# Optimization experiments

Measured on AMD Instinct MI355X. Metric: run time of the kernel, lower is better.

Reference implementation:

```python
import jax, jax.numpy as jnp
import numpy as np

B, T_ENC, T_DEC = 32, 256, 256
ENC, HID, ATT, CCH, K = 512, 1024, 128, 32, 31
OUT, PRE = 80, 256
ZONEOUT = 0.1
P_DROP = 0.5
PAD = (K - 1) // 2


def setup_inputs() -> dict:
    key = jax.random.key(0)
    ks = jax.random.split(key, 20)
    def n(k, shape, s=0.02):
        return jax.random.normal(k, shape, dtype=jnp.float32) * s
    inp = {}
    inp["encoder_outs"] = jax.random.normal(ks[0], (B, T_ENC, ENC), dtype=jnp.float32)
    inp["decoder_targets"] = jax.random.normal(ks[1], (B, T_DEC, OUT), dtype=jnp.float32)
    keep = 1.0 - P_DROP
    # pre-sampled inverted-dropout masks for the 2 prenet layers at every step
    inp["prenet_masks"] = jax.random.bernoulli(ks[2], keep, (T_DEC, 2, B, PRE)).astype(jnp.float32) / keep
    inp["in_lens"] = jax.random.randint(ks[3], (B,), T_ENC // 2, T_ENC + 1, dtype=jnp.int32)
    # location-sensitive attention params
    inp["V_w"] = n(ks[4], (ATT, ENC)); inp["V_b"] = jnp.zeros((ATT,), jnp.float32)
    inp["W_w"] = n(ks[5], (ATT, HID))
    inp["U_w"] = n(ks[6], (ATT, CCH))
    inp["F_w"] = n(ks[7], (CCH, 1, K))
    inp["w_w"] = n(ks[8], (1, ATT)); inp["w_b"] = jnp.zeros((1,), jnp.float32)
    # prenet
    inp["pre_w0"] = n(ks[9], (PRE, OUT)); inp["pre_b0"] = jnp.zeros((PRE,), jnp.float32)
    inp["pre_w1"] = n(ks[10], (PRE, PRE)); inp["pre_b1"] = jnp.zeros((PRE,), jnp.float32)
    # stacked LSTM cells (zoneout wrappers)
    inp["l0_wih"] = n(ks[11], (4 * HID, ENC + PRE)); inp["l0_whh"] = n(ks[12], (4 * HID, HID))
    inp["l0_bih"] = jnp.zeros((4 * HID,), jnp.float32); inp["l0_bhh"] = jnp.zeros((4 * HID,), jnp.float32)
    inp["l1_wih"] = n(ks[13], (4 * HID, HID)); inp["l1_whh"] = n(ks[14], (4 * HID, HID))
    inp["l1_bih"] = jnp.zeros((4 * HID,), jnp.float32); inp["l1_bhh"] = jnp.zeros((4 * HID,), jnp.float32)
    # output projections
    inp["feat_w"] = n(ks[15], (OUT, ENC + HID))
    inp["prob_w"] = n(ks[16], (1, ENC + HID)); inp["prob_b"] = jnp.zeros((1,), jnp.float32)
    return inp


def _lstm_cell(x, h, c, wih, whh, bih, bhh):
    g = x @ wih.T + bih + h @ whh.T + bhh
    i, f, gg, o = jnp.split(g, 4, axis=1)  # torch LSTMCell gate order
    c2 = jax.nn.sigmoid(f) * c + jax.nn.sigmoid(i) * jnp.tanh(gg)
    h2 = jax.nn.sigmoid(o) * jnp.tanh(c2)
    return h2, c2


def _decode(encoder_outs, decoder_targets, prenet_masks, in_lens,
            V_w, V_b, W_w, U_w, F_w, w_w, w_b,
            pre_w0, pre_b0, pre_w1, pre_b1,
            l0_wih, l0_whh, l0_bih, l0_bhh,
            l1_wih, l1_whh, l1_bih, l1_bhh,
            feat_w, prob_w, prob_b):
    b = encoder_outs.shape[0]
    pad_mask = jnp.arange(T_ENC)[None, :] >= in_lens[:, None]       # [B,T_enc] True = pad
    att_uniform = (~pad_mask).astype(jnp.float32) / in_lens[:, None].astype(jnp.float32)
    processed_memory = encoder_outs @ V_w.T + V_b                   # [B,T_enc,ATT]
    neg = jnp.float32(-1e9)

    # teacher forcing: prev_out at step 0 is the go-frame, then target[t-1]
    targets_prev = jnp.concatenate(
        [jnp.zeros((b, 1, OUT), jnp.float32), decoder_targets[:, :-1]], axis=1)
    xs = (jnp.swapaxes(targets_prev, 0, 1), prenet_masks[:, 0], prenet_masks[:, 1],
          jnp.arange(T_DEC))

    def step(carry, x):
        h0, c0, h1, c1, cum = carry
        prev_out, m0, m1, t = x
        # location-sensitive attention (prev_att_w = None at t=0 -> uniform over valid)
        att_prev = jnp.where(t == 0, att_uniform, cum)              # [B,T_enc]
        f = jax.lax.conv_general_dilated(
            att_prev[:, None, :], F_w, (1,), [(PAD, PAD)],
            dimension_numbers=("NCH", "OIH", "NCH"))                # [B,CCH,T_enc]
        f = jnp.swapaxes(f, 1, 2)                                   # [B,T_enc,CCH]
        erg = jnp.tanh(processed_memory + (h0 @ W_w.T)[:, None, :] + f @ U_w.T)
        erg = (erg @ w_w.T + w_b)[..., 0]                           # [B,T_enc]
        erg = jnp.where(pad_mask, neg, erg)
        aw = jax.nn.softmax(erg, axis=1)
        att_c = jnp.einsum("bt,bte->be", aw, encoder_outs)          # [B,ENC]
        # prenet (dropout always on, via pre-sampled masks)
        p = jax.nn.relu(prev_out @ pre_w0.T + pre_b0) * m0
        p = jax.nn.relu(p @ pre_w1.T + pre_b1) * m1
        xin = jnp.concatenate([att_c, p], axis=1)
        # zoneout LSTM stack (eval-mode zoneout: convex mix of prev/new states)
        h0n, c0n = _lstm_cell(xin, h0, c0, l0_wih, l0_whh, l0_bih, l0_bhh)
        h0 = ZONEOUT * h0 + (1.0 - ZONEOUT) * h0n
        c0 = ZONEOUT * c0 + (1.0 - ZONEOUT) * c0n
        h1n, c1n = _lstm_cell(h0, h1, c1, l1_wih, l1_whh, l1_bih, l1_bhh)
        h1 = ZONEOUT * h1 + (1.0 - ZONEOUT) * h1n
        c1 = ZONEOUT * c1 + (1.0 - ZONEOUT) * c1n
        hcs = jnp.concatenate([h1, att_c], axis=1)                  # [B,HID+ENC]
        out = hcs @ feat_w.T                                        # [B,OUT] (no bias)
        logit = hcs @ prob_w.T + prob_b                             # [B,1]
        return (h0, c0, h1, c1, cum + aw), (out, logit, aw)

    z = jnp.zeros((b, HID), jnp.float32)
    carry0 = (z, z, z, z, jnp.zeros((b, T_ENC), jnp.float32))
    _, (outs, logits, att_ws) = jax.lax.scan(step, carry0, xs)
    outs = jnp.transpose(outs, (1, 2, 0))      # [B,OUT,T_dec]
    logits = logits[..., 0].T                  # [B,T_dec]
    att_ws = jnp.swapaxes(att_ws, 0, 1)        # [B,T_dec,T_enc]
    return outs, logits, att_ws


def reference(encoder_outs, decoder_targets, prenet_masks, in_lens,
              V_w, V_b, W_w, U_w, F_w, w_w, w_b,
              pre_w0, pre_b0, pre_w1, pre_b1,
              l0_wih, l0_whh, l0_bih, l0_bhh,
              l1_wih, l1_whh, l1_bih, l1_bhh,
              feat_w, prob_w, prob_b):
    return _decode(encoder_outs, decoder_targets, prenet_masks, in_lens,
                   V_w, V_b, W_w, U_w, F_w, w_w, w_b,
                   pre_w0, pre_b0, pre_w1, pre_b1,
                   l0_wih, l0_whh, l0_bih, l0_bhh,
                   l1_wih, l1_whh, l1_bih, l1_bhh,
                   feat_w, prob_w, prob_b)
```

## Files before the change

### kernel.cpp

```cpp
#include <hip/hip_runtime.h>

typedef _Float16 half2_t __attribute__((ext_vector_type(2)));
typedef unsigned uint_t;

#define B_    32
#define TE_   256
#define TD_   256
#define ENC_  512
#define HID_  1024
#define ATT_  128
#define OUT_  80
#define PRE_  256

#define LOG_OFF  655360u
#define ATTW_OFF 663552u

#define OFF_PM    0u
#define OFF_P1H   1048576u
#define OFF_M     2097152u
#define OFF_WWHT  2101248u
#define OFF_ENCH  2166784u
#define OFF_W0P   4263936u
#define OFF_W1P   7933952u
#define OFF_XC0   12128256u
#define OFF_XC1   12173312u
#define OFF_C0    12206080u
#define OFF_C1    12238848u
#define OFF_CUM   12271616u
#define OFF_ATTC  12279808u
#define OFF_END   12328960u

__device__ __forceinline__ float rcp_f(float x){ return __builtin_amdgcn_rcpf(x); }
__device__ __forceinline__ float sigm(float x){ return rcp_f(1.0f + __expf(-x)); }
__device__ __forceinline__ float tanh_f(float x){ float e = __expf(2.0f*x); return 1.0f - 2.0f*rcp_f(e+1.0f); }

__device__ __forceinline__ uint_t packh2(float a, float b){
  half2_t h; h[0] = (_Float16)a; h[1] = (_Float16)b;
  return __builtin_bit_cast(uint_t, h);
}
__device__ __forceinline__ float dot2f(uint_t w, uint_t x, float c){
#if __has_builtin(__builtin_amdgcn_fdot2)
  return __builtin_amdgcn_fdot2(__builtin_bit_cast(half2_t, w),
                                __builtin_bit_cast(half2_t, x), c, false);
#else
  half2_t a = __builtin_bit_cast(half2_t, w), b = __builtin_bit_cast(half2_t, x);
  return c + (float)a[0]*(float)b[0] + (float)a[1]*(float)b[1];
#endif
}


__global__ void k_init(float* __restrict__ ws){
  unsigned n = OFF_END - OFF_XC0;
  for (unsigned i = blockIdx.x*blockDim.x + threadIdx.x; i < n; i += gridDim.x*blockDim.x)
    ws[OFF_XC0 + i] = 0.f;
}

__global__ void k_precm(const float* __restrict__ Uw, const float* __restrict__ Fw,
                        float* __restrict__ ws){
  float* M = ws + OFF_M;
  for (int idx = threadIdx.x; idx < 128*31; idx += blockDim.x){
    int a = idx / 31, k = idx % 31;
    float s = 0.f;
    for (int c = 0; c < 32; c++) s += Uw[a*32+c]*Fw[c*31+k];
    M[idx] = s;
  }
}

__global__ void k_cvtww(const float* __restrict__ Ww, float* __restrict__ ws){
  uint_t* WT = (uint_t*)(ws + OFF_WWHT);
  int p = blockIdx.x;
  for (int a = threadIdx.x; a < 128; a += blockDim.x)
    WT[p*128 + a] = packh2(Ww[a*1024 + 2*p], Ww[a*1024 + 2*p + 1]);
}

__global__ void k_packenc(const float* __restrict__ enc, float* __restrict__ ws){
  uint_t* ENCH = (uint_t*)(ws + OFF_ENCH);
  size_t row = blockIdx.x;
  for (int j = threadIdx.x; j < 256; j += blockDim.x)
    ENCH[row*256 + j] = packh2(enc[row*512 + 2*j], enc[row*512 + 2*j + 1]);
}

__global__ void k_packw0(const float* __restrict__ wih, const float* __restrict__ whh,
                         float* __restrict__ ws){
  uint_t* W = (uint_t*)(ws + OFF_W0P);
  size_t r = blockIdx.x;
  for (int p = threadIdx.x; p < 896; p += blockDim.x){
    int k = 2*p;
    const float* src = (k < 768) ? (wih + r*768 + k) : (whh + r*1024 + (k-768));
    W[r*896 + p] = packh2(src[0], src[1]);
  }
}

__global__ void k_packw1(const float* __restrict__ wih, const float* __restrict__ whh,
                         float* __restrict__ ws){
  uint_t* W = (uint_t*)(ws + OFF_W1P);
  size_t r = blockIdx.x;
  for (int p = threadIdx.x; p < 1024; p += blockDim.x){
    int k = 2*p;
    const float* src = (k < 1024) ? (wih + r*1024 + k) : (whh + r*1024 + (k-1024));
    W[r*1024 + p] = packh2(src[0], src[1]);
  }
}

__global__ __launch_bounds__(256) void k_pm(const float* __restrict__ enc,
    const float* __restrict__ Vw, const float* __restrict__ Vb, float* __restrict__ ws){
  float* pm = ws + OFF_PM;
  int b  = blockIdx.x >> 2;
  int s0 = (blockIdx.x & 3) << 6;
  int a  = threadIdx.x & 127;
  int sh = threadIdx.x >> 7;
  __shared__ float Vl[128*65];
  __shared__ float El[64*64];
  float acc[32];
  #pragma unroll
  for (int i=0;i<32;i++) acc[i]=0.f;
  for (int kc=0; kc<ENC_; kc+=64){
    for (int i=threadIdx.x; i<128*64; i+=256){
      int aa = i>>6, kk = i&63;
      Vl[aa*65+kk] = Vw[aa*ENC_ + kc + kk];
    }
    for (int i=threadIdx.x; i<64*64; i+=256){
      int ss = i>>6, kk = i&63;
      El[i] = enc[(size_t)(b*TE_ + s0 + ss)*ENC_ + kc + kk];
    }
    __syncthreads();
    for (int k=0;k<64;k++){
      float va = Vl[a*65+k];
      const float* er = &El[(sh*32)*64 + k];
      #pragma unroll
      for (int s=0;s<32;s++) acc[s] += va * er[s*64];
    }
    __syncthreads();
  }
  float bb = Vb[a];
  for (int s=0;s<32;s++)
    pm[((size_t)b*128 + a)*256 + (s0 + sh*32 + s)] = acc[s] + bb;
}

__global__ __launch_bounds__(256) void k_pre(const float* __restrict__ tgt,
    const float* __restrict__ w0, const float* __restrict__ b0,
    const float* __restrict__ w1, const float* __restrict__ b1,
    const float* __restrict__ masks, float* __restrict__ ws){
  uint_t* P1H = (uint_t*)(ws + OFF_P1H);
  int t = blockIdx.x, j = threadIdx.x;
  __shared__ float xl[32*80];
  __shared__ float p0l[32*256];
  __shared__ float p1s[256*32];
  for (int i=j; i<32*80; i+=256){
    int b = i/80, o = i%80;
    xl[i] = (t==0) ? 0.f : tgt[((size_t)b*TD_ + (t-1))*80 + o];
  }
  __syncthreads();
  {
    float bj = b0[j];
    float w[80];
    #pragma unroll
    for (int o=0;o<80;o++) w[o] = w0[j*80+o];
    for (int b=0;b<32;b++){
      float a0=0,a1=0,a2=0,a3=0;
      const float* x = &xl[b*80];
      #pragma unroll
      for (int o=0;o<80;o+=4){
        a0+=w[o]*x[o]; a1+=w[o+1]*x[o+1]; a2+=w[o+2]*x[o+2]; a3+=w[o+3]*x[o+3];
      }
      float m = masks[(((size_t)t*2+0)*32+b)*256 + j];
      p0l[b*256 + j] = fmaxf(bj+a0+a1+a2+a3, 0.f) * m;
    }
  }
  __syncthreads();
  {
    float bj = b1[j];
    const float4* wr = (const float4*)(w1 + j*256);
    float acc[32];
    #pragma unroll
    for (int i=0;i<32;i++) acc[i]=0.f;
    for (int o4=0;o4<64;o4++){
      float4 w = wr[o4];
      #pragma unroll
      for (int b=0;b<32;b++){
        const float4 xv = *(const float4*)&p0l[b*256 + o4*4];
        acc[b] += w.x*xv.x + w.y*xv.y + w.z*xv.z + w.w*xv.w;
      }
    }
    for (int b=0;b<32;b++){
      float m = masks[(((size_t)t*2+1)*32+b)*256 + j];
      p1s[j*32 + b] = fmaxf(bj+acc[b], 0.f) * m;
    }
  }
  __syncthreads();
  for (int i=j; i<32*128; i+=256){
    int b = i >> 7, jp = i & 127;
    P1H[((size_t)t*32 + b)*128 + jp] = packh2(p1s[(2*jp)*32 + b], p1s[(2*jp+1)*32 + b]);
  }
}


__global__ __launch_bounds__(512) void k_stepa(int t,
    const int* __restrict__ lens, const float* __restrict__ ww, const float* __restrict__ wb,
    const float* __restrict__ featw, const float* __restrict__ probw,
    const float* __restrict__ probb, float* __restrict__ ws, float* __restrict__ out){
  __shared__ __align__(16) uint_t h0l[512];
  __shared__ __align__(16) float Ml[128*32];
  __shared__ __align__(16) float apad[320];
  __shared__ __align__(16) float whl[128];
  __shared__ __align__(16) float wl[128];
  __shared__ __align__(16) float scl[256];
  __shared__ __align__(16) float awl[256];
  __shared__ __align__(16) float redl[128];
  __shared__ __align__(16) float psq[2048];
  __shared__ __align__(16) float redo[512];
  const int blk = blockIdx.x, tid = threadIdx.x;
  const int pc = t & 1, pp = pc ^ 1;
  uint_t* XC0 = (uint_t*)(ws + OFF_XC0);
  uint_t* XC1 = (uint_t*)(ws + OFF_XC1);
  float* ATTC = ws + OFF_ATTC;

  if (blk >= 32){
    if (t < 2) return;
    const int tt = t - 2;
    int ob = blk - 32;
    int b = tid & 31, rr = (tid>>5)&3, ksq = tid>>7;
    int r = ob*4 + rr;
    const float* wr = (r < 80) ? (featw + (size_t)r*1536) : probw;
    const float* acp = ATTC + (size_t)(tt%3)*16384 + b*512;
    float acc = 0.f;
    for (int j=0;j<96;j++){
      int k = ksq*384 + j*4;
      float x0,x1,x2,x3;
      if (k < 1024){
        uint2 hw = *(const uint2*)(XC1 + b*1024 + pc*512 + (k>>1));
        half2_t ha = __builtin_bit_cast(half2_t, hw.x);
        half2_t hb = __builtin_bit_cast(half2_t, hw.y);
        x0 = (float)ha[0]; x1 = (float)ha[1]; x2 = (float)hb[0]; x3 = (float)hb[1];
      } else {
        float4 f = *(const float4*)(acp + (k-1024));
        x0 = f.x; x1 = f.y; x2 = f.z; x3 = f.w;
      }
      if (r <= 80){
        float4 wv = *(const float4*)(wr + k);
        acc += wv.x*x0 + wv.y*x1 + wv.z*x2 + wv.w*x3;
      }
    }
    redo[(rr*4+ksq)*32 + b] = acc;
    __syncthreads();
    if (tid < 128){
      int b2 = tid&31, r2 = tid>>5;
      float vsum = redo[(r2*4+0)*32+b2] + redo[(r2*4+1)*32+b2]
                 + redo[(r2*4+2)*32+b2] + redo[(r2*4+3)*32+b2];
      int rr2 = ob*4 + r2;
      if (rr2 < 80)       out[((size_t)b2*80 + rr2)*256 + tt] = vsum;
      else if (rr2 == 80) out[LOG_OFF + (size_t)b2*256 + tt] = vsum + probb[0];
    }
    return;
  }

  if (t >= TD_) return;
  const int b = blk;
  const int len = lens[b];
  const float* PM = ws + OFF_PM;
  const float* Mg = ws + OFF_M;
  const uint_t* WWHT = (const uint_t*)(ws + OFF_WWHT);
  const uint_t* ENCH = (const uint_t*)(ws + OFF_ENCH);
  const uint_t* P1H = (const uint_t*)(ws + OFF_P1H);
  float* CUM = ws + OFF_CUM;

  if (tid < 128)
    *(uint4*)(h0l + tid*4) = *(const uint4*)(XC0 + b*1408 + 384 + pp*512 + tid*4);
  for (int i=tid; i<128*31; i+=512) Ml[(i/31)*32 + (i%31)] = Mg[i];
  for (int i=tid; i<288; i+=512){
    int p = i - 15;
    float vv = 0.f;
    if (p >= 0 && p < 256)
      vv = (t==0) ? ((p < len) ? 1.0f/(float)len : 0.f) : CUM[b*256 + p];
    apad[i] = vv;
  }
  if (tid < 128) wl[tid] = ww[tid];
  __syncthreads();
  {
    int aW = tid & 127, qW = tid >> 7;
    const uint_t* wt = WWHT + (size_t)(qW*128)*128 + aW;
    const uint_t* hb = h0l + qW*128;
    float s0 = 0.f, s1 = 0.f;
    #pragma unroll 8
    for (int p=0;p<128;p+=2){
      s0 = dot2f(wt[(size_t)p*128],     hb[p],   s0);
      s1 = dot2f(wt[(size_t)(p+1)*128], hb[p+1], s1);
    }
    psq[qW*128 + aW] = s0 + s1;
  }
  __syncthreads();
  if (tid < 128) whl[tid] = psq[tid] + psq[128+tid] + psq[256+tid] + psq[384+tid];
  __syncthreads();
  {
    int pg = tid & 63, q = tid >> 6;
    float apw[36];
    #pragma unroll
    for (int i=0;i<36;i+=4) *(float4*)&apw[i] = *(const float4*)&apad[pg*4 + i];
    float part0=0, part1=0, part2=0, part3=0;
    const float* pmb = PM + (size_t)b*128*256;
    for (int aa=0; aa<16; aa++){
      int a = q*16 + aa;
      const float* mr = Ml + a*32;
      float4 pv = *(const float4*)(pmb + (size_t)a*256 + pg*4);
      float wa = whl[a];
      float u0 = pv.x + wa, u1 = pv.y + wa, u2 = pv.z + wa, u3 = pv.w + wa;
      #pragma unroll
      for (int k=0;k<28;k+=4){
        float4 m4 = *(const float4*)(mr + k);
        u0 += m4.x*apw[k]   + m4.y*apw[k+1] + m4.z*apw[k+2] + m4.w*apw[k+3];
        u1 += m4.x*apw[k+1] + m4.y*apw[k+2] + m4.z*apw[k+3] + m4.w*apw[k+4];
        u2 += m4.x*apw[k+2] + m4.y*apw[k+3] + m4.z*apw[k+4] + m4.w*apw[k+5];
        u3 += m4.x*apw[k+3] + m4.y*apw[k+4] + m4.z*apw[k+5] + m4.w*apw[k+6];
      }
      float m28 = mr[28], m29 = mr[29], m30 = mr[30];
      u0 += m28*apw[28] + m29*apw[29] + m30*apw[30];
      u1 += m28*apw[29] + m29*apw[30] + m30*apw[31];
      u2 += m28*apw[30] + m29*apw[31] + m30*apw[32];
      u3 += m28*apw[31] + m29*apw[32] + m30*apw[33];
      float wv = wl[a];
      part0 += tanh_f(u0)*wv; part1 += tanh_f(u1)*wv;
      part2 += tanh_f(u2)*wv; part3 += tanh_f(u3)*wv;
    }
    float4 pp2; pp2.x = part0; pp2.y = part1; pp2.z = part2; pp2.w = part3;
    *(float4*)&psq[tid*4] = pp2;
  }
  __syncthreads();
  if (tid < 256){
    float s = wb[0];
    int pgg = tid >> 2, d = tid & 3;
    #pragma unroll
    for (int qq=0;qq<8;qq++) s += psq[(qq*64 + pgg)*4 + d];
    scl[tid] = (tid >= len) ? -1.0e9f : s;
  }
  __syncthreads();
  if (tid < 128) redl[tid] = fmaxf(scl[tid], scl[tid+128]);
  __syncthreads();
  if (tid < 64){
    float v = fmaxf(redl[tid], redl[tid+64]);
    #pragma unroll
    for (int off=32; off>0; off>>=1) v = fmaxf(v, __shfl_down(v, off));
    if (tid==0) redl[0] = v;
  }
  __syncthreads();
  float mx = redl[0];
  if (tid < 256) awl[tid] = __expf(scl[tid]-mx);
  __syncthreads();
  if (tid < 128) redl[tid] = awl[tid] + awl[tid+128];
  __syncthreads();
  if (tid < 64){
    float v = redl[tid] + redl[tid+64];
    #pragma unroll
    for (int off=32; off>0; off>>=1) v += __shfl_down(v, off);
    if (tid==0) redl[0] = v;
  }
  __syncthreads();
  float inv = rcp_f(redl[0]);
  if (tid < 256){
    float aw = awl[tid]*inv;
    awl[tid] = aw;
    CUM[b*256 + tid] += aw;
    out[ATTW_OFF + ((size_t)b*TD_ + t)*256 + tid] = aw;
  }
  __syncthreads();
  {
    int el = tid & 127, ph = tid >> 7;
    const uint_t* ep = ENCH + ((size_t)b*256 + ph*64)*256 + el*2;
    float c0=0,c1=0,c2=0,c3=0;
    for (int p=0;p<64;p++){
      float a = awl[ph*64 + p];
      uint2 ev = *(const uint2*)(ep + (size_t)p*256);
      half2_t h0v = __builtin_bit_cast(half2_t, ev.x);
      half2_t h1v = __builtin_bit_cast(half2_t, ev.y);
      c0 += a*(float)h0v[0]; c1 += a*(float)h0v[1];
      c2 += a*(float)h1v[0]; c3 += a*(float)h1v[1];
    }
    float4 ca; ca.x=c0; ca.y=c1; ca.z=c2; ca.w=c3;
    *(float4*)&psq[(ph*128 + el)*4] = ca;
  }
  __syncthreads();
  if (tid < 128){
    float4 s = *(const float4*)&psq[tid*4];
    #pragma unroll
    for (int g=1; g<4; g++){
      float4 o = *(const float4*)&psq[(g*128+tid)*4];
      s.x+=o.x; s.y+=o.y; s.z+=o.z; s.w+=o.w;
    }
    *(float4*)(ATTC + (size_t)(t%3)*16384 + b*512 + tid*4) = s;
    XC0[b*1408 + tid*2]     = packh2(s.x, s.y);
    XC0[b*1408 + tid*2 + 1] = packh2(s.z, s.w);
    XC0[b*1408 + 256 + tid] = P1H[((size_t)t*32 + b)*128 + tid];
  }
}


__global__ __launch_bounds__(512) void k_stepb(int t,
    const float* __restrict__ l0bih, const float* __restrict__ l0bhh,
    const float* __restrict__ l1bih, const float* __restrict__ l1bhh,
    float* __restrict__ ws){
  __shared__ __align__(16) uint_t lds[16*1028 + 32*132];
  uint_t* wlds = lds;
  uint_t* xl   = lds + 16*1028;
  float*  gs   = (float*)lds;
  const int tid = threadIdx.x;
  const int pc = t & 1, pp = pc ^ 1;
  const int bp = tid & 15, ul = (tid>>4)&3, kq = tid>>6;
  const int sb = tid >> 4, sp = (tid & 15) * 8;
  const bool is0 = blockIdx.x < 256;
  const int u0 = (is0 ? blockIdx.x : blockIdx.x - 256) * 4;
  uint_t* XC0 = (uint_t*)(ws + OFF_XC0);
  uint_t* XC1 = (uint_t*)(ws + OFF_XC1);
  _Float16* XC0h = (_Float16*)XC0;
  _Float16* XC1h = (_Float16*)XC1;

  if (is0){
    if (t >= TD_) return;
    const uint_t* W0P = (const uint_t*)(ws + OFF_W0P);
    for (int i=tid; i<16*896; i+=512){
      int r = i/896, p = i - r*896;
      wlds[r*904 + p] = W0P[(size_t)((r&3)*1024 + u0 + (r>>2))*896 + p];
    }
    float a0[4]={0,0,0,0}, a1[4]={0,0,0,0};
    uint4 rx0, rx1;
    { const uint_t* src = XC0 + sb*1408 + sp;
      rx0 = *(const uint4*)src; rx1 = *(const uint4*)(src+4); }
    #pragma unroll 1
    for (int c=0;c<7;c++){
      __syncthreads();
      *(uint4*)(xl + sb*132 + sp)     = rx0;
      *(uint4*)(xl + sb*132 + sp + 4) = rx1;
      __syncthreads();
      if (c+1 < 7){
        int co = (c+1)*128 + sp;
        const uint_t* src = (co < 384) ? (XC0 + sb*1408 + co)
                                       : (XC0 + sb*1408 + 384 + pp*512 + (co-384));
        rx0 = *(const uint4*)src; rx1 = *(const uint4*)(src+4);
      }
      const int wb = c*128 + kq*16;
      const uint_t* xpa = xl + bp*132 + kq*16;
      const uint_t* xpb = xl + (bp+16)*132 + kq*16;
      uint2 xa[8], xb[8];
      #pragma unroll
      for (int j=0;j<8;j++){ xa[j] = *(const uint2*)(xpa + 2*j); xb[j] = *(const uint2*)(xpb + 2*j); }
      #pragma unroll
      for (int g=0; g<4; g++){
        const uint_t* wr = wlds + (g + 4*ul)*904 + wb;
        float s0 = a0[g], s1 = a1[g];
        #pragma unroll
        for (int j=0;j<8;j++){
          uint2 w = *(const uint2*)(wr + 2*j);
          s0 = dot2f(w.x, xa[j].x, s0); s0 = dot2f(w.y, xa[j].y, s0);
          s1 = dot2f(w.x, xb[j].x, s1); s1 = dot2f(w.y, xb[j].y, s1);
        }
        a0[g] = s0; a1[g] = s1;
      }
    }
    __syncthreads();
    #pragma unroll
    for (int g=0; g<4; g++){
      gs[(kq*16 + g + 4*ul)*33 + bp]      = a0[g];
      gs[(kq*16 + g + 4*ul)*33 + bp + 16] = a1[g];
    }
    __syncthreads();
    if (tid < 128){
      int b = tid & 31, uu = tid >> 5;
      int u = u0 + uu;
      float g4[4];
      #pragma unroll
      for (int g=0; g<4; g++){
        float s = 0.f;
        #pragma unroll
        for (int k2=0;k2<8;k2++) s += gs[(k2*16 + g + 4*uu)*33 + b];
        g4[g] = s + l0bih[g*1024+u] + l0bhh[g*1024+u];
      }
      float c_old = (ws + OFF_C0)[u*32 + b];
      float h_old = (float)XC0h[b*2816 + 768 + pp*1024 + u];
      float cn = sigm(g4[1])*c_old + sigm(g4[0])*tanh_f(g4[2]);
      float hn = sigm(g4[3])*tanh_f(cn);
      (ws + OFF_C0)[u*32 + b] = 0.1f*c_old + 0.9f*cn;
      XC0h[b*2816 + 768 + pc*1024 + u] = (_Float16)(0.1f*h_old + 0.9f*hn);
    }
  } else {
    if (t < 1) return;
    const uint_t* W1P = (const uint_t*)(ws + OFF_W1P);
    for (int i=tid; i<16*1024; i+=512){
      int r = i >> 10, p = i & 1023;
      wlds[r*1028 + p] = W1P[(size_t)((r&3)*1024 + u0 + (r>>2))*1024 + p];
    }
    float a0[4]={0,0,0,0}, a1[4]={0,0,0,0};
    uint4 rx0, rx1;
    { const uint_t* src = XC0 + sb*1408 + 384 + pp*512 + sp;
      rx0 = *(const uint4*)src; rx1 = *(const uint4*)(src+4); }
    #pragma unroll 1
    for (int c=0;c<8;c++){
      __syncthreads();
      *(uint4*)(xl + sb*132 + sp)     = rx0;
      *(uint4*)(xl + sb*132 + sp + 4) = rx1;
      __syncthreads();
      if (c+1 < 8){
        int co = (c+1)*128 + sp;
        const uint_t* src = (co < 512) ? (XC0 + sb*1408 + 384 + pp*512 + co)
                                       : (XC1 + sb*1024 + pc*512 + (co-512));
        rx0 = *(const uint4*)src; rx1 = *(const uint4*)(src+4);
      }
      const int wb = c*128 + kq*16;
      const uint_t* xpa = xl + bp*132 + kq*16;
      const uint_t* xpb = xl + (bp+16)*132 + kq*16;
      uint2 xa[8], xb[8];
      #pragma unroll
      for (int j=0;j<8;j++){ xa[j] = *(const uint2*)(xpa + 2*j); xb[j] = *(const uint2*)(xpb + 2*j); }
      #pragma unroll
      for (int g=0; g<4; g++){
        const uint_t* wr = wlds + (g + 4*ul)*1028 + wb;
        float s0 = a0[g], s1 = a1[g];
        #pragma unroll
        for (int j=0;j<8;j++){
          uint2 w = *(const uint2*)(wr + 2*j);
          s0 = dot2f(w.x, xa[j].x, s0); s0 = dot2f(w.y, xa[j].y, s0);
          s1 = dot2f(w.x, xb[j].x, s1); s1 = dot2f(w.y, xb[j].y, s1);
        }
        a0[g] = s0; a1[g] = s1;
      }
    }
    __syncthreads();
    #pragma unroll
    for (int g=0; g<4; g++){
      gs[(kq*16 + g + 4*ul)*33 + bp]      = a0[g];
      gs[(kq*16 + g + 4*ul)*33 + bp + 16] = a1[g];
    }
    __syncthreads();
    if (tid < 128){
      int b = tid & 31, uu = tid >> 5;
      int u = u0 + uu;
      float g4[4];
      #pragma unroll
      for (int g=0; g<4; g++){
        float s = 0.f;
        #pragma unroll
        for (int k2=0;k2<8;k2++) s += gs[(k2*16 + g + 4*uu)*33 + b];
        g4[g] = s + l1bih[g*1024+u] + l1bhh[g*1024+u];
      }
      float c_old = (ws + OFF_C1)[u*32 + b];
      float h_old = (float)XC1h[b*2048 + pc*1024 + u];
      float cn = sigm(g4[1])*c_old + sigm(g4[0])*tanh_f(g4[2]);
      float hn = sigm(g4[3])*tanh_f(cn);
      (ws + OFF_C1)[u*32 + b] = 0.1f*c_old + 0.9f*cn;
      XC1h[b*2048 + pp*1024 + u] = (_Float16)(0.1f*h_old + 0.9f*hn);
    }
  }
}

extern "C" void kernel_launch(void* const* d_in, const int* in_sizes, int n_in,
                              void* d_out, int out_size, void* d_ws, size_t ws_size,
                              hipStream_t stream){
  const float* enc   = (const float*)d_in[0];
  const float* tgt   = (const float*)d_in[1];
  const float* masks = (const float*)d_in[2];
  const int*   lens  = (const int*)  d_in[3];
  const float* Vw    = (const float*)d_in[4];
  const float* Vb    = (const float*)d_in[5];
  const float* Ww    = (const float*)d_in[6];
  const float* Uw    = (const float*)d_in[7];
  const float* Fw    = (const float*)d_in[8];
  const float* ww    = (const float*)d_in[9];
  const float* wb    = (const float*)d_in[10];
  const float* pw0   = (const float*)d_in[11];
  const float* pb0   = (const float*)d_in[12];
  const float* pw1   = (const float*)d_in[13];
  const float* pb1   = (const float*)d_in[14];
  const float* l0wih = (const float*)d_in[15];
  const float* l0whh = (const float*)d_in[16];
  const float* l0bih = (const float*)d_in[17];
  const float* l0bhh = (const float*)d_in[18];
  const float* l1wih = (const float*)d_in[19];
  const float* l1whh = (const float*)d_in[20];
  const float* l1bih = (const float*)d_in[21];
  const float* l1bhh = (const float*)d_in[22];
  const float* featw = (const float*)d_in[23];
  const float* probw = (const float*)d_in[24];
  const float* probb = (const float*)d_in[25];
  float* ws  = (float*)d_ws;
  float* out = (float*)d_out;

  k_init   <<<256, 256,0,stream>>>(ws);
  k_pre    <<<256, 256,0,stream>>>(tgt, pw0, pb0, pw1, pb1, masks, ws);
  k_precm  <<<1,   256,0,stream>>>(Uw, Fw, ws);
  k_cvtww  <<<512, 128,0,stream>>>(Ww, ws);
  k_packenc<<<8192,256,0,stream>>>(enc, ws);
  k_packw0 <<<4096,256,0,stream>>>(l0wih, l0whh, ws);
  k_packw1 <<<4096,256,0,stream>>>(l1wih, l1whh, ws);
  k_pm     <<<128, 256,0,stream>>>(enc, Vw, Vb, ws);

  for (int t = 0; t < TD_; t++){
    k_stepa<<<56, 512,0,stream>>>(t, lens, ww, wb, featw, probw, probb, ws, out);
    k_stepb<<<512,512,0,stream>>>(t, l0bih, l0bhh, l1bih, l1bhh, ws);
  }
  k_stepb<<<512,512,0,stream>>>(256, l0bih, l0bhh, l1bih, l1bhh, ws);
  k_stepa<<<56, 512,0,stream>>>(256, lens, ww, wb, featw, probw, probb, ws, out);
  k_stepa<<<56, 512,0,stream>>>(257, lens, ww, wb, featw, probw, probb, ws, out);
}
```

Before: 15.92 ms.

## Merge LSTM layer blocks into one block and prefetch weights into registers

The separate layer-0 and layer-1 LSTM blocks become one block per 4 hidden units that runs both layers in turn, halving the grid to 256 blocks. All weights for both layers, along with biases and old cell and hidden states, are loaded into registers at kernel start so the global loads overlap. The activation chunks are double-buffered in LDS with a two-ahead register prefetch, which removes one barrier per chunk, and the LDS reads are widened to 128 bits. In exchange each block does serial work for both layers and carries heavy register pressure (15 uint4 of weights per thread), with launch bounds set to one block per CU.

```diff
diff --git a/kernel.cpp b/kernel.cpp
--- a/kernel.cpp
+++ b/kernel.cpp
@@ -393,67 +393,125 @@
 }
 
 
-__global__ __launch_bounds__(512) void k_stepb(int t,
+#define W0S 908
+#define W1S 1028
+#define LW1 14528u
+#define LXB0 30976u
+#define LXB1 35200u
+#define LTOT 39424u
+
+__global__ __launch_bounds__(512, 1) void k_stepb(int t,
     const float* __restrict__ l0bih, const float* __restrict__ l0bhh,
     const float* __restrict__ l1bih, const float* __restrict__ l1bhh,
     float* __restrict__ ws){
-  __shared__ __align__(16) uint_t lds[16*1028 + 32*132];
-  uint_t* wlds = lds;
-  uint_t* xl   = lds + 16*1028;
-  float*  gs   = (float*)lds;
+  __shared__ __align__(16) uint_t lds[LTOT];
+  uint_t* w0l = lds;
+  uint_t* w1l = lds + LW1;
+  float*  gs  = (float*)(lds + LW1);
   const int tid = threadIdx.x;
   const int pc = t & 1, pp = pc ^ 1;
   const int bp = tid & 15, ul = (tid>>4)&3, kq = tid>>6;
-  const int sb = tid >> 4, sp = (tid & 15) * 8;
-  const bool is0 = blockIdx.x < 256;
-  const int u0 = (is0 ? blockIdx.x : blockIdx.x - 256) * 4;
+  const int sb = tid >> 4, sp = (tid & 15)*8;
+  const int u0 = blockIdx.x*4;
   uint_t* XC0 = (uint_t*)(ws + OFF_XC0);
   uint_t* XC1 = (uint_t*)(ws + OFF_XC1);
   _Float16* XC0h = (_Float16*)XC0;
   _Float16* XC1h = (_Float16*)XC1;
-
-  if (is0){
-    if (t >= TD_) return;
-    const uint_t* W0P = (const uint_t*)(ws + OFF_W0P);
-    for (int i=tid; i<16*896; i+=512){
-      int r = i/896, p = i - r*896;
-      wlds[r*904 + p] = W0P[(size_t)((r&3)*1024 + u0 + (r>>2))*896 + p];
-    }
-    float a0[4]={0,0,0,0}, a1[4]={0,0,0,0};
-    uint4 rx0, rx1;
-    { const uint_t* src = XC0 + sb*1408 + sp;
-      rx0 = *(const uint4*)src; rx1 = *(const uint4*)(src+4); }
-    #pragma unroll 1
+  float* C0 = ws + OFF_C0;
+  float* C1 = ws + OFF_C1;
+  const uint_t* W0P = (const uint_t*)(ws + OFF_W0P);
+  const uint_t* W1P = (const uint_t*)(ws + OFF_W1P);
+
+  uint4 w0r[7], w1r[8];
+  #pragma unroll
+  for (int q=0;q<7;q++){
+    int i = q*512 + tid;
+    int r = i/224, c4 = i - r*224;
+    w0r[q] = *(const uint4*)(W0P + (size_t)((r&3)*1024 + u0 + (r>>2))*896 + c4*4);
+  }
+  #pragma unroll
+  for (int q=0;q<8;q++){
+    int i = q*512 + tid;
+    int r = i>>8, c4 = i&255;
+    w1r[q] = *(const uint4*)(W1P + (size_t)((r&3)*1024 + u0 + (r>>2))*1024 + c4*4);
+  }
+  float b0s[4], b1s[4], c0old=0.f, c1old=0.f, h0old=0.f, h1old=0.f;
+  {
+    int bb = tid & 31, uu = (tid >> 5) & 3;
+    int u = u0 + uu;
+    if (tid < 128){
+      #pragma unroll
+      for (int g=0;g<4;g++){
+        b0s[g] = l0bih[g*1024+u] + l0bhh[g*1024+u];
+        b1s[g] = l1bih[g*1024+u] + l1bhh[g*1024+u];
+      }
+      c0old = C0[u*32 + bb];
+      c1old = C1[u*32 + bb];
+      h0old = (float)XC0h[bb*2816 + 768 + pp*1024 + u];
+      h1old = (float)XC1h[bb*2048 + pc*1024 + u];
+    }
+  }
+
+  float a0[4]={0,0,0,0}, a1[4]={0,0,0,0};
+
+  if (t < TD_){
+    uint4 rA0,rA1,rB0,rB1;
+    { const uint_t* s = XC0 + sb*1408 + sp;                       rA0=*(const uint4*)s; rA1=*(const uint4*)(s+4); }
+    { const uint_t* s = XC0 + sb*1408 + 128 + sp;                 rB0=*(const uint4*)s; rB1=*(const uint4*)(s+4); }
+    #pragma unroll
+    for (int q=0;q<7;q++){
+      int i = q*512 + tid;
+      int r = i/224, c4 = i - r*224;
+      *(uint4*)(w0l + r*W0S + c4*4) = w0r[q];
+    }
+    *(uint4*)(lds + LXB0 + sb*132 + sp) = rA0;
+    *(uint4*)(lds + LXB0 + sb*132 + sp + 4) = rA1;
+    rA0 = rB0; rA1 = rB1;
+    { const uint_t* s = XC0 + sb*1408 + 256 + sp;                 rB0=*(const uint4*)s; rB1=*(const uint4*)(s+4); }
+    #pragma unroll
     for (int c=0;c<7;c++){
       __syncthreads();
-      *(uint4*)(xl + sb*132 + sp)     = rx0;
-      *(uint4*)(xl + sb*132 + sp + 4) = rx1;
-      __syncthreads();
       if (c+1 < 7){
-        int co = (c+1)*128 + sp;
-        const uint_t* src = (co < 384) ? (XC0 + sb*1408 + co)
+        uint_t* xw = lds + ((c&1) ? LXB0 : LXB1);
+        *(uint4*)(xw + sb*132 + sp)     = rA0;
+        *(uint4*)(xw + sb*132 + sp + 4) = rA1;
+        rA0 = rB0; rA1 = rB1;
+        if (c+3 < 7){
+          int co = (c+3)*128 + sp;
+          const uint_t* s = (co < 384) ? (XC0 + sb*1408 + co)
                                        : (XC0 + sb*1408 + 384 + pp*512 + (co-384));
-        rx0 = *(const uint4*)src; rx1 = *(const uint4*)(src+4);
-      }
-      const int wb = c*128 + kq*16;
-      const uint_t* xpa = xl + bp*132 + kq*16;
-      const uint_t* xpb = xl + (bp+16)*132 + kq*16;
-      uint2 xa[8], xb[8];
-      #pragma unroll
-      for (int j=0;j<8;j++){ xa[j] = *(const uint2*)(xpa + 2*j); xb[j] = *(const uint2*)(xpb + 2*j); }
+          rB0 = *(const uint4*)s; rB1 = *(const uint4*)(s+4);
+        }
+      }
+      const uint_t* xr = lds + ((c&1) ? LXB1 : LXB0);
+      const uint_t* xpa = xr + bp*132 + kq*16;
+      const uint_t* xpb = xr + (bp+16)*132 + kq*16;
+      uint4 xa[4], xbv[4];
+      #pragma unroll
+      for (int j4=0;j4<4;j4++){ xa[j4] = *(const uint4*)(xpa + 4*j4); xbv[j4] = *(const uint4*)(xpb + 4*j4); }
+      const int wb_ = c*128 + kq*16;
       #pragma unroll
       for (int g=0; g<4; g++){
-        const uint_t* wr = wlds + (g + 4*ul)*904 + wb;
+        const uint_t* wr = w0l + (g + 4*ul)*W0S + wb_;
         float s0 = a0[g], s1 = a1[g];
         #pragma unroll
-        for (int j=0;j<8;j++){
-          uint2 w = *(const uint2*)(wr + 2*j);
-          s0 = dot2f(w.x, xa[j].x, s0); s0 = dot2f(w.y, xa[j].y, s0);
-          s1 = dot2f(w.x, xb[j].x, s1); s1 = dot2f(w.y, xb[j].y, s1);
+        for (int j4=0;j4<4;j4++){
+          uint4 w = *(const uint4*)(wr + 4*j4);
+          s0 = dot2f(w.x, xa[j4].x, s0); s0 = dot2f(w.y, xa[j4].y, s0);
+          s0 = dot2f(w.z, xa[j4].z, s0); s0 = dot2f(w.w, xa[j4].w, s0);
+          s1 = dot2f(w.x, xbv[j4].x, s1); s1 = dot2f(w.y, xbv[j4].y, s1);
+          s1 = dot2f(w.z, xbv[j4].z, s1); s1 = dot2f(w.w, xbv[j4].w, s1);
         }
         a0[g] = s0; a1[g] = s1;
       }
     }
+  }
+  uint4 pA0=make_uint4(0,0,0,0), pA1=pA0, pB0=pA0, pB1=pA0;
+  if (t >= 1){
+    { const uint_t* s = XC0 + sb*1408 + 384 + pp*512 + sp;        pA0=*(const uint4*)s; pA1=*(const uint4*)(s+4); }
+    { const uint_t* s = XC0 + sb*1408 + 384 + pp*512 + 128 + sp;  pB0=*(const uint4*)s; pB1=*(const uint4*)(s+4); }
+  }
+  if (t < TD_){
     __syncthreads();
     #pragma unroll
     for (int g=0; g<4; g++){
@@ -462,89 +520,95 @@
     }
     __syncthreads();
     if (tid < 128){
-      int b = tid & 31, uu = tid >> 5;
+      int bb = tid & 31, uu = tid >> 5;
       int u = u0 + uu;
       float g4[4];
       #pragma unroll
       for (int g=0; g<4; g++){
         float s = 0.f;
         #pragma unroll
-        for (int k2=0;k2<8;k2++) s += gs[(k2*16 + g + 4*uu)*33 + b];
-        g4[g] = s + l0bih[g*1024+u] + l0bhh[g*1024+u];
-      }
-      float c_old = (ws + OFF_C0)[u*32 + b];
-      float h_old = (float)XC0h[b*2816 + 768 + pp*1024 + u];
-      float cn = sigm(g4[1])*c_old + sigm(g4[0])*tanh_f(g4[2]);
+        for (int k2=0;k2<8;k2++) s += gs[(k2*16 + g + 4*uu)*33 + bb];
+        g4[g] = s + b0s[g];
+      }
+      float cn = sigm(g4[1])*c0old + sigm(g4[0])*tanh_f(g4[2]);
       float hn = sigm(g4[3])*tanh_f(cn);
-      (ws + OFF_C0)[u*32 + b] = 0.1f*c_old + 0.9f*cn;
-      XC0h[b*2816 + 768 + pc*1024 + u] = (_Float16)(0.1f*h_old + 0.9f*hn);
-    }
-  } else {
-    if (t < 1) return;
-    const uint_t* W1P = (const uint_t*)(ws + OFF_W1P);
-    for (int i=tid; i<16*1024; i+=512){
-      int r = i >> 10, p = i & 1023;
-      wlds[r*1028 + p] = W1P[(size_t)((r&3)*1024 + u0 + (r>>2))*1024 + p];
-    }
-    float a0[4]={0,0,0,0}, a1[4]={0,0,0,0};
-    uint4 rx0, rx1;
-    { const uint_t* src = XC0 + sb*1408 + 384 + pp*512 + sp;
-      rx0 = *(const uint4*)src; rx1 = *(const uint4*)(src+4); }
-    #pragma unroll 1
+      C0[u*32 + bb] = 0.1f*c0old + 0.9f*cn;
+      XC0h[bb*2816 + 768 + pc*1024 + u] = (_Float16)(0.1f*h0old + 0.9f*hn);
+    }
+  }
+
+  if (t >= 1){
+    __syncthreads();
+    #pragma unroll
+    for (int q=0;q<8;q++){
+      int i = q*512 + tid;
+      int r = i>>8, c4 = i&255;
+      *(uint4*)(w1l + r*W1S + c4*4) = w1r[q];
+    }
+    *(uint4*)(lds + LXB0 + sb*132 + sp)     = pA0;
+    *(uint4*)(lds + LXB0 + sb*132 + sp + 4) = pA1;
+    pA0 = pB0; pA1 = pB1;
+    { const uint_t* s = XC0 + sb*1408 + 384 + pp*512 + 256 + sp;  pB0=*(const uint4*)s; pB1=*(const uint4*)(s+4); }
+    float e0[4]={0,0,0,0}, e1[4]={0,0,0,0};
+    #pragma unroll
     for (int c=0;c<8;c++){
       __syncthreads();
-      *(uint4*)(xl + sb*132 + sp)     = rx0;
-      *(uint4*)(xl + sb*132 + sp + 4) = rx1;
-      __syncthreads();
       if (c+1 < 8){
-        int co = (c+1)*128 + sp;
-        const uint_t* src = (co < 512) ? (XC0 + sb*1408 + 384 + pp*512 + co)
+        uint_t* xw = lds + ((c&1) ? LXB0 : LXB1);
+        *(uint4*)(xw + sb*132 + sp)     = pA0;
+        *(uint4*)(xw + sb*132 + sp + 4) = pA1;
+        pA0 = pB0; pA1 = pB1;
+        if (c+3 < 8){
+          int co = (c+3)*128 + sp;
+          const uint_t* s = (co < 512) ? (XC0 + sb*1408 + 384 + pp*512 + co)
                                        : (XC1 + sb*1024 + pc*512 + (co-512));
-        rx0 = *(const uint4*)src; rx1 = *(const uint4*)(src+4);
-      }
-      const int wb = c*128 + kq*16;
-      const uint_t* xpa = xl + bp*132 + kq*16;
-      const uint_t* xpb = xl + (bp+16)*132 + kq*16;
-      uint2 xa[8], xb[8];
-      #pragma unroll
-      for (int j=0;j<8;j++){ xa[j] = *(const uint2*)(xpa + 2*j); xb[j] = *(const uint2*)(xpb + 2*j); }
+          pB0 = *(const uint4*)s; pB1 = *(const uint4*)(s+4);
+        }
+      }
+      const uint_t* xr = lds + ((c&1) ? LXB1 : LXB0);
+      const uint_t* xpa = xr + bp*132 + kq*16;
+      const uint_t* xpb = xr + (bp+16)*132 + kq*16;
+      uint4 xa[4], xbv[4];
+      #pragma unroll
+      for (int j4=0;j4<4;j4++){ xa[j4] = *(const uint4*)(xpa + 4*j4); xbv[j4] = *(const uint4*)(xpb + 4*j4); }
+      const int wb_ = c*128 + kq*16;
       #pragma unroll
       for (int g=0; g<4; g++){
-        const uint_t* wr = wlds + (g + 4*ul)*1028 + wb;
-        float s0 = a0[g], s1 = a1[g];
+        const uint_t* wr = w1l + (g + 4*ul)*W1S + wb_;
+        float s0 = e0[g], s1 = e1[g];
         #pragma unroll
-        for (int j=0;j<8;j++){
-          uint2 w = *(const uint2*)(wr + 2*j);
-          s0 = dot2f(w.x, xa[j].x, s0); s0 = dot2f(w.y, xa[j].y, s0);
-          s1 = dot2f(w.x, xb[j].x, s1); s1 = dot2f(w.y, xb[j].y, s1);
+        for (int j4=0;j4<4;j4++){
+          uint4 w = *(const uint4*)(wr + 4*j4);
+          s0 = dot2f(w.x, xa[j4].x, s0); s0 = dot2f(w.y, xa[j4].y, s0);
+          s0 = dot2f(w.z, xa[j4].z, s0); s0 = dot2f(w.w, xa[j4].w, s0);
+          s1 = dot2f(w.x, xbv[j4].x, s1); s1 = dot2f(w.y, xbv[j4].y, s1);
+          s1 = dot2f(w.z, xbv[j4].z, s1); s1 = dot2f(w.w, xbv[j4].w, s1);
         }
-        a0[g] = s0; a1[g] = s1;
+        e0[g] = s0; e1[g] = s1;
       }
     }
     __syncthreads();
     #pragma unroll
     for (int g=0; g<4; g++){
-      gs[(kq*16 + g + 4*ul)*33 + bp]      = a0[g];
-      gs[(kq*16 + g + 4*ul)*33 + bp + 16] = a1[g];
+      gs[(kq*16 + g + 4*ul)*33 + bp]      = e0[g];
+      gs[(kq*16 + g + 4*ul)*33 + bp + 16] = e1[g];
     }
     __syncthreads();
     if (tid < 128){
-      int b = tid & 31, uu = tid >> 5;
+      int bb = tid & 31, uu = tid >> 5;
       int u = u0 + uu;
       float g4[4];
       #pragma unroll
       for (int g=0; g<4; g++){
         float s = 0.f;
         #pragma unroll
-        for (int k2=0;k2<8;k2++) s += gs[(k2*16 + g + 4*uu)*33 + b];
-        g4[g] = s + l1bih[g*1024+u] + l1bhh[g*1024+u];
-      }
-      float c_old = (ws + OFF_C1)[u*32 + b];
-      float h_old = (float)XC1h[b*2048 + pc*1024 + u];
-      float cn = sigm(g4[1])*c_old + sigm(g4[0])*tanh_f(g4[2]);
+        for (int k2=0;k2<8;k2++) s += gs[(k2*16 + g + 4*uu)*33 + bb];
+        g4[g] = s + b1s[g];
+      }
+      float cn = sigm(g4[1])*c1old + sigm(g4[0])*tanh_f(g4[2]);
       float hn = sigm(g4[3])*tanh_f(cn);
-      (ws + OFF_C1)[u*32 + b] = 0.1f*c_old + 0.9f*cn;
-      XC1h[b*2048 + pp*1024 + u] = (_Float16)(0.1f*h_old + 0.9f*hn);
+      C1[u*32 + bb] = 0.1f*c1old + 0.9f*cn;
+      XC1h[bb*2048 + pp*1024 + u] = (_Float16)(0.1f*h1old + 0.9f*hn);
     }
   }
 }
@@ -592,9 +656,9 @@
 
   for (int t = 0; t < TD_; t++){
     k_stepa<<<56, 512,0,stream>>>(t, lens, ww, wb, featw, probw, probb, ws, out);
-    k_stepb<<<512,512,0,stream>>>(t, l0bih, l0bhh, l1bih, l1bhh, ws);
-  }
-  k_stepb<<<512,512,0,stream>>>(256, l0bih, l0bhh, l1bih, l1bhh, ws);
+    k_stepb<<<256,512,0,stream>>>(t, l0bih, l0bhh, l1bih, l1bhh, ws);
+  }
+  k_stepb<<<256,512,0,stream>>>(256, l0bih, l0bhh, l1bih, l1bhh, ws);
   k_stepa<<<56, 512,0,stream>>>(256, lens, ww, wb, featw, probw, probb, ws, out);
   k_stepa<<<56, 512,0,stream>>>(257, lens, ww, wb, featw, probw, probb, ws, out);
 }
```

New measurement: 16.49 ms. 3.6% more time.
